# Kernel optimization log

Hardware: AMD Instinct MI355X
Metric: run time of the kernel (lower is better)

## Reference

```python
import jax, jax.numpy as jnp
import numpy as np
from jax import lax

SQRT2 = 1.4142135623730951
NEG_SLOPE = 0.2


def _haar_kernels():
    l = np.ones((1, 2), np.float32) / np.float32(np.sqrt(2.0))
    h = l.copy()
    h[0, 0] = -h[0, 0]
    ll = l.T @ l
    lh = h.T @ l
    hl = l.T @ h
    hh = h.T @ h
    return (jnp.asarray(ll), jnp.asarray(lh), jnp.asarray(hl), jnp.asarray(hh))


def _blur_kernel():
    k = np.array([1.0, 3.0, 3.0, 1.0], np.float32)
    K = np.outer(k, k)
    K /= K.sum()
    return jnp.asarray(K)


def upfirdn2d(x, kernel, up=1, down=1, pad=(0, 0, 0, 0)):
    # x: [B,C,H,W]; depthwise FIR matching StyleGAN2 upfirdn2d semantics:
    # upsample by zero-insertion (up-1 zeros AFTER each sample), pad, true
    # convolution (kernel flipped, since lax does cross-correlation), then
    # stride-`down` decimation. Trailing zeros of torch's upsampling are
    # folded into the right/bottom pad (+up-1).
    B, C, H, W = x.shape
    px0, px1, py0, py1 = pad
    w = jnp.flip(kernel, (0, 1))[None, None].astype(x.dtype)  # [1,1,kh,kw]
    y = lax.conv_general_dilated(
        x.reshape(B * C, 1, H, W), w,
        window_strides=(down, down),
        padding=((py0, py1 + up - 1), (px0, px1 + up - 1)),
        lhs_dilation=(up, up),
        dimension_numbers=('NCHW', 'OIHW', 'NCHW'))
    return y.reshape(B, C, y.shape[2], y.shape[3])


def setup_inputs() -> dict:
    key = jax.random.key(0)
    k1, k2, k3 = jax.random.split(key, 3)
    x = jax.random.normal(k1, (8, 16, 512, 512), dtype=jnp.float32)
    conv_w = jax.random.normal(k2, (512, 16, 1, 1), dtype=jnp.float32)
    conv_b = jax.random.normal(k3, (512,), dtype=jnp.float32) * 0.1
    return {"x": x, "conv_w": conv_w, "conv_b": conv_b}


def reference(x, conv_w, conv_b):
    ll, lh, hl, hh = _haar_kernels()
    # ---- InverseHaarTransform(4): 16ch [B,16,H,W] -> 4ch [B,4,2H,2W] ----
    xll, xlh, xhl, xhh = jnp.split(x, 4, axis=1)
    p = (1, 0, 1, 0)
    inv = (upfirdn2d(xll, ll, up=2, pad=p)
           + upfirdn2d(xlh, -lh, up=2, pad=p)
           + upfirdn2d(xhl, -hl, up=2, pad=p)
           + upfirdn2d(xhh, hh, up=2, pad=p))
    # ---- Downsample(blur_kernel=[1,3,3,1]): [B,4,2H,2W] -> [B,4,H,W] ----
    bk = _blur_kernel()
    pp = bk.shape[0] - 2  # p = len(kernel) - factor
    pad0, pad1 = (pp + 1) // 2, pp // 2
    dwn = upfirdn2d(inv, bk, down=2, pad=(pad0, pad1, pad0, pad1))
    # ---- HaarTransform(4): [B,4,H,W] -> [B,16,H/2,W/2] ----
    new_in = jnp.concatenate(
        [upfirdn2d(dwn, k, down=2, pad=(0, 0, 0, 0)) for k in (ll, lh, hl, hh)],
        axis=1)
    # ---- ConvLayer: EqualConv2d 1x1 (no bias) + FusedLeakyReLU ----
    fan_in = conv_w.shape[1] * conv_w.shape[2] * conv_w.shape[3]
    scale = 1.0 / float(np.sqrt(fan_in))
    out = jnp.einsum('bchw,oc->bohw', new_in, conv_w[:, :, 0, 0] * scale)
    out = out + conv_b[None, :, None, None]
    out = jnp.where(out >= 0, out, NEG_SLOPE * out) * SQRT2
    return (new_in, out)
```

## Files before the change

### kernel.cpp

```cpp
#include <hip/hip_runtime.h>


#define H_IN 512
#define W_IN 512
#define H_OUT 256
#define W_OUT 256
#define NB 8
#define C_MID 16
#define C_OUT 512

typedef float fx4 __attribute__((ext_vector_type(4)));

__device__ __forceinline__ float cL(int fsel, float a0, float a1, float a2, float a3) {
  return fsel == 0 ? (a0 + 7.f*a1 + 7.f*a2 + a3) : (a0 + a1 - a2 - a3);
}
__device__ __forceinline__ float cH(int fsel, float a0, float a1, float a2, float a3) {
  return fsel == 0 ? (a0 + 5.f*a1 - 5.f*a2 - a3) : (a0 - a1 - a2 + a3);
}

__device__ __forceinline__ fx4 vfma(fx4 v, float s, fx4 a) {
  a.x = fmaf(v.x, s, a.x); a.y = fmaf(v.y, s, a.y);
  a.z = fmaf(v.z, s, a.z); a.w = fmaf(v.w, s, a.w);
  return a;
}

__global__ __launch_bounds__(256) void k_fused(const float* __restrict__ x,
                                               const float* __restrict__ w,
                                               const float* __restrict__ bias,
                                               float* __restrict__ nin,
                                               float* __restrict__ out) {
  __shared__ fx4 ws4[C_OUT * 4];
  __shared__ float bs[C_OUT];
  const int t = threadIdx.x;

  const fx4* w4 = reinterpret_cast<const fx4*>(w);
  const float wscale = 0.25f * (1.f / 256.f);
#pragma unroll
  for (int i = 0; i < 8; ++i) ws4[t + 256 * i] = w4[t + 256 * i] * wscale;
  bs[t] = bias[t];
  bs[t + 256] = bias[t + 256];

  const int q = t & 63;
  const int y = blockIdx.x * 4 + (t >> 6);
  const int b = blockIdx.y;
  const int y0 = 2 * y - 1;

  const float WL[2][4] = {{1.f, 7.f, 7.f, 1.f}, {1.f, 1.f, -1.f, -1.f}};
  const float WH[2][4] = {{1.f, 5.f, -5.f, -1.f}, {1.f, -1.f, -1.f, 1.f}};

  fx4 acc[16];
#pragma unroll
  for (int c = 0; c < 16; ++c) acc[c] = (fx4){0.f, 0.f, 0.f, 0.f};

#pragma unroll
  for (int ch = 0; ch < 4; ++ch) {
#pragma unroll
    for (int g = 0; g < 4; ++g) {
      const int gY = g & 1, gX = g >> 1;
      const float sg = (g == 1 || g == 2) ? -1.f : 1.f;
      const float* xp = x + (size_t)(b * 16 + g * 4 + ch) * (H_IN * W_IN);
#pragma unroll
      for (int p = 0; p < 4; ++p) {
        const int yy = y0 + p;
        if (yy < 0 || yy >= H_IN) continue;
        const float* row = xp + (size_t)yy * W_IN + 8 * q;
        float c0 = (q > 0) ? row[-1] : 0.f;
        const fx4 m0 = *reinterpret_cast<const fx4*>(row);
        const fx4 m1 = *reinterpret_cast<const fx4*>(row + 4);
        const float c9 = (q < 63) ? row[8] : 0.f;
        const float cc[10] = {c0, m0.x, m0.y, m0.z, m0.w,
                              m1.x, m1.y, m1.z, m1.w, c9};
        const float wl = sg * WL[gY][p];
        const float wh = sg * WH[gY][p];
        fx4 vL, vH;
        vL.x = cL(gX, cc[0], cc[1], cc[2], cc[3]);
        vL.y = cL(gX, cc[2], cc[3], cc[4], cc[5]);
        vL.z = cL(gX, cc[4], cc[5], cc[6], cc[7]);
        vL.w = cL(gX, cc[6], cc[7], cc[8], cc[9]);
        vH.x = cH(gX, cc[0], cc[1], cc[2], cc[3]);
        vH.y = cH(gX, cc[2], cc[3], cc[4], cc[5]);
        vH.z = cH(gX, cc[4], cc[5], cc[6], cc[7]);
        vH.w = cH(gX, cc[6], cc[7], cc[8], cc[9]);
        acc[0 * 4 + ch] = vfma(vL, wl, acc[0 * 4 + ch]);
        acc[1 * 4 + ch] = vfma(vL, wh, acc[1 * 4 + ch]);
        acc[2 * 4 + ch] = vfma(vH, wl, acc[2 * 4 + ch]);
        acc[3 * 4 + ch] = vfma(vH, wh, acc[3 * 4 + ch]);
      }
    }
  }

  const float inv = 1.f / 256.f;
#pragma unroll
  for (int c = 0; c < 16; ++c) {
    fx4 r;
    r.x = acc[c].x * inv; r.y = acc[c].y * inv;
    r.z = acc[c].z * inv; r.w = acc[c].w * inv;
    *reinterpret_cast<fx4*>(
        nin + ((size_t)(b * C_MID + c) * H_OUT + y) * W_OUT + 4 * q) = r;
  }

  __syncthreads();

  float* op = out + ((size_t)(b * C_OUT) * H_OUT + y) * W_OUT + 4 * q;
  const float s2 = 1.41421356237309515f;
#pragma unroll 2
  for (int o = 0; o < C_OUT; ++o) {
    const fx4 w0 = ws4[4*o], w1 = ws4[4*o+1], w2 = ws4[4*o+2], w3 = ws4[4*o+3];
    const float bo = bs[o];
    fx4 a; a.x = bo; a.y = bo; a.z = bo; a.w = bo;
    a = vfma(acc[0],  w0.x, a); a = vfma(acc[1],  w0.y, a);
    a = vfma(acc[2],  w0.z, a); a = vfma(acc[3],  w0.w, a);
    a = vfma(acc[4],  w1.x, a); a = vfma(acc[5],  w1.y, a);
    a = vfma(acc[6],  w1.z, a); a = vfma(acc[7],  w1.w, a);
    a = vfma(acc[8],  w2.x, a); a = vfma(acc[9],  w2.y, a);
    a = vfma(acc[10], w2.z, a); a = vfma(acc[11], w2.w, a);
    a = vfma(acc[12], w3.x, a); a = vfma(acc[13], w3.y, a);
    a = vfma(acc[14], w3.z, a); a = vfma(acc[15], w3.w, a);
    a.x = (a.x >= 0.f ? a.x : 0.2f * a.x) * s2;
    a.y = (a.y >= 0.f ? a.y : 0.2f * a.y) * s2;
    a.z = (a.z >= 0.f ? a.z : 0.2f * a.z) * s2;
    a.w = (a.w >= 0.f ? a.w : 0.2f * a.w) * s2;
    __builtin_nontemporal_store(a,
        reinterpret_cast<fx4*>(op + (size_t)o * (H_OUT * W_OUT)));
  }
}

extern "C" void kernel_launch(void* const* d_in, const int* in_sizes, int n_in,
                              void* d_out, int out_size, void* d_ws, size_t ws_size,
                              hipStream_t stream) {
  const float* x    = (const float*)d_in[0];
  const float* w    = (const float*)d_in[1];
  const float* bias = (const float*)d_in[2];
  float* nin = (float*)d_out;
  float* out = (float*)d_out + (size_t)NB * C_MID * H_OUT * W_OUT;

  k_fused<<<dim3(64, 8), dim3(256), 0, stream>>>(x, w, bias, nin, out);
}
```

Measured before the change: 267.5 us.

## Prepack scaled weights in a prep kernel and read them as uniform scalar loads

Adds a small prep kernel that pre-scales the conv weights, folds the sqrt2 gain into weights and bias, and packs them into a 32-float stride in the workspace. The fused kernel drops its shared-memory weight staging and barrier and reads the uniform weights from global memory, where they may become scalar loads. Halo pixels now come from wavefront shuffles instead of extra global loads, and the leaky-ReLU becomes an fmax. The nin stores become nontemporal. The cost is an extra kernel launch and reliance on the compiler to scalarize the weight reads.

Result: faster. 249.1 us (-6.9%).

```diff
diff --git a/kernel.cpp b/kernel.cpp
--- a/kernel.cpp
+++ b/kernel.cpp
@@ -24,22 +24,22 @@
   return a;
 }
 
+__global__ __launch_bounds__(256) void k_prep(const float* __restrict__ w,
+                                              const float* __restrict__ bias,
+                                              float* __restrict__ wpk) {
+  const int o = blockIdx.x * 256 + threadIdx.x;
+  const float s2 = 1.41421356237309515f;
+  const float wscale = s2 * 0.25f * (1.f / 256.f);
+#pragma unroll
+  for (int c = 0; c < 16; ++c) wpk[o * 32 + c] = w[o * 16 + c] * wscale;
+  wpk[o * 32 + 16] = bias[o] * s2;
+}
+
 __global__ __launch_bounds__(256) void k_fused(const float* __restrict__ x,
-                                               const float* __restrict__ w,
-                                               const float* __restrict__ bias,
+                                               const float* __restrict__ wpk,
                                                float* __restrict__ nin,
                                                float* __restrict__ out) {
-  __shared__ fx4 ws4[C_OUT * 4];
-  __shared__ float bs[C_OUT];
   const int t = threadIdx.x;
-
-  const fx4* w4 = reinterpret_cast<const fx4*>(w);
-  const float wscale = 0.25f * (1.f / 256.f);
-#pragma unroll
-  for (int i = 0; i < 8; ++i) ws4[t + 256 * i] = w4[t + 256 * i] * wscale;
-  bs[t] = bias[t];
-  bs[t + 256] = bias[t + 256];
-
   const int q = t & 63;
   const int y = blockIdx.x * 4 + (t >> 6);
   const int b = blockIdx.y;
@@ -64,12 +64,14 @@
         const int yy = y0 + p;
         if (yy < 0 || yy >= H_IN) continue;
         const float* row = xp + (size_t)yy * W_IN + 8 * q;
-        float c0 = (q > 0) ? row[-1] : 0.f;
         const fx4 m0 = *reinterpret_cast<const fx4*>(row);
         const fx4 m1 = *reinterpret_cast<const fx4*>(row + 4);
-        const float c9 = (q < 63) ? row[8] : 0.f;
-        const float cc[10] = {c0, m0.x, m0.y, m0.z, m0.w,
-                              m1.x, m1.y, m1.z, m1.w, c9};
+        const float c0s = __shfl(m1.w, q - 1);
+        const float c9s = __shfl(m0.x, q + 1);
+        const float cc0 = (q > 0) ? c0s : 0.f;
+        const float cc9 = (q < 63) ? c9s : 0.f;
+        const float cc[10] = {cc0, m0.x, m0.y, m0.z, m0.w,
+                              m1.x, m1.y, m1.z, m1.w, cc9};
         const float wl = sg * WL[gY][p];
         const float wh = sg * WH[gY][p];
         fx4 vL, vH;
@@ -95,31 +97,22 @@
     fx4 r;
     r.x = acc[c].x * inv; r.y = acc[c].y * inv;
     r.z = acc[c].z * inv; r.w = acc[c].w * inv;
-    *reinterpret_cast<fx4*>(
-        nin + ((size_t)(b * C_MID + c) * H_OUT + y) * W_OUT + 4 * q) = r;
+    __builtin_nontemporal_store(r, reinterpret_cast<fx4*>(
+        nin + ((size_t)(b * C_MID + c) * H_OUT + y) * W_OUT + 4 * q));
   }
 
-  __syncthreads();
-
   float* op = out + ((size_t)(b * C_OUT) * H_OUT + y) * W_OUT + 4 * q;
-  const float s2 = 1.41421356237309515f;
 #pragma unroll 2
   for (int o = 0; o < C_OUT; ++o) {
-    const fx4 w0 = ws4[4*o], w1 = ws4[4*o+1], w2 = ws4[4*o+2], w3 = ws4[4*o+3];
-    const float bo = bs[o];
+    const float* __restrict__ wrow = wpk + (o << 5);
+    const float bo = wrow[16];
     fx4 a; a.x = bo; a.y = bo; a.z = bo; a.w = bo;
-    a = vfma(acc[0],  w0.x, a); a = vfma(acc[1],  w0.y, a);
-    a = vfma(acc[2],  w0.z, a); a = vfma(acc[3],  w0.w, a);
-    a = vfma(acc[4],  w1.x, a); a = vfma(acc[5],  w1.y, a);
-    a = vfma(acc[6],  w1.z, a); a = vfma(acc[7],  w1.w, a);
-    a = vfma(acc[8],  w2.x, a); a = vfma(acc[9],  w2.y, a);
-    a = vfma(acc[10], w2.z, a); a = vfma(acc[11], w2.w, a);
-    a = vfma(acc[12], w3.x, a); a = vfma(acc[13], w3.y, a);
-    a = vfma(acc[14], w3.z, a); a = vfma(acc[15], w3.w, a);
-    a.x = (a.x >= 0.f ? a.x : 0.2f * a.x) * s2;
-    a.y = (a.y >= 0.f ? a.y : 0.2f * a.y) * s2;
-    a.z = (a.z >= 0.f ? a.z : 0.2f * a.z) * s2;
-    a.w = (a.w >= 0.f ? a.w : 0.2f * a.w) * s2;
+#pragma unroll
+    for (int c = 0; c < 16; ++c) a = vfma(acc[c], wrow[c], a);
+    a.x = fmaxf(a.x, 0.2f * a.x);
+    a.y = fmaxf(a.y, 0.2f * a.y);
+    a.z = fmaxf(a.z, 0.2f * a.z);
+    a.w = fmaxf(a.w, 0.2f * a.w);
     __builtin_nontemporal_store(a,
         reinterpret_cast<fx4*>(op + (size_t)o * (H_OUT * W_OUT)));
   }
@@ -133,6 +126,8 @@
   const float* bias = (const float*)d_in[2];
   float* nin = (float*)d_out;
   float* out = (float*)d_out + (size_t)NB * C_MID * H_OUT * W_OUT;
+  float* wpk = (float*)d_ws;
 
-  k_fused<<<dim3(64, 8), dim3(256), 0, stream>>>(x, w, bias, nin, out);
+  k_prep<<<dim3(2), dim3(256), 0, stream>>>(w, bias, wpk);
+  k_fused<<<dim3(64, 8), dim3(256), 0, stream>>>(x, wpk, nin, out);
 }
```
